# Kernel tuning notes

Hardware: AMD Instinct MI355X
Metric: run time of the kernel (lower is better)

## Reference

```python
import jax, jax.numpy as jnp
import numpy as np

B = 4; E_PER = 100_000; E = B * E_PER
N_NODES = 50_000; N_REL = 500; D = 64; D_LG = 256
K_PER_VI = 20; S_VI = E // K_PER_VI          # 20000 sorted vi segments
S_VJ_PER = 5_000; S_VJ = B * S_VJ_PER        # 20000 unsorted vj segments
N_MEM = 131_072
INTERACT = ((0, 3), (0, 2, 3), (0, 4), (0, 2, 4), (1, 3), (1, 2, 3), (1, 4), (1, 2, 4))


def _build_edges():
    rng = np.random.default_rng(0)
    idx_vi = np.repeat(np.arange(S_VI), K_PER_VI)          # sorted segment ids
    gpb = S_VI // B
    eg = idx_vi // gpb                                     # sorted by eg_idx too
    vi = rng.integers(0, N_NODES, S_VI)[idx_vi]
    idx_vj = np.empty(E, dtype=np.int64)
    for b in range(B):
        loc = np.concatenate([np.arange(S_VJ_PER), rng.integers(0, S_VJ_PER, E_PER - S_VJ_PER)])
        rng.shuffle(loc)
        idx_vj[b * E_PER:(b + 1) * E_PER] = b * S_VJ_PER + loc  # every group non-empty
    vj = rng.integers(0, N_NODES, S_VJ)[idx_vj]            # consistent (eg, vj) per group
    rel = rng.integers(0, N_REL, E)
    e2vi = rng.integers(0, N_MEM, E)
    e2vj = rng.integers(0, N_MEM, E)
    return np.stack([eg, vi, vj, rel, idx_vi, idx_vj, e2vi, e2vj], axis=1).astype(np.int32)


def setup_inputs() -> dict:
    key = jax.random.key(0)
    ks = jax.random.split(key, 10)
    return {
        "node_attention": jax.random.uniform(ks[0], (B, N_NODES), jnp.float32),
        "scanned_edges": jnp.asarray(_build_edges()),
        "edges_y": jax.random.uniform(ks[1], (E,), jnp.float32),
        "hidden_uncon": jax.random.normal(ks[2], (1, N_NODES, D_LG), jnp.float32),
        "hidden_con": jax.random.normal(ks[3], (N_MEM, D), jnp.float32),
        "Wc": jax.random.normal(ks[4], (D, D), jnp.float32) / np.sqrt(D).astype(np.float32),
        "bc": jnp.zeros((D,), jnp.float32),
        "Wu": jax.random.normal(ks[5], (D_LG, D), jnp.float32) / np.sqrt(D_LG).astype(np.float32),
        "bu": jnp.zeros((D,), jnp.float32),
        "rel_table": jax.random.normal(ks[6], (N_REL, D), jnp.float32) * 0.05,
        "ws": jax.random.normal(ks[7], (len(INTERACT), D), jnp.float32) / np.sqrt(float(len(INTERACT))).astype(np.float32) if False else jax.random.normal(ks[7], (len(INTERACT), D), jnp.float32) * (1.0 / np.sqrt(len(INTERACT)).astype(np.float32)),
        "fb": jnp.zeros((D,), jnp.float32),
        "out_w": jax.random.normal(ks[8], (D,), jnp.float32),
        "out_b": jnp.zeros((D,), jnp.float32),
        "n_vi_segments": S_VI,
        "n_vj_segments": S_VJ,
    }


def reference(node_attention, scanned_edges, edges_y, hidden_uncon, hidden_con,
              Wc, bc, Wu, bu, rel_table, ws, fb, out_w, out_b,
              n_vi_segments, n_vj_segments):
    eg, vi, vj, rel = (scanned_edges[:, i] for i in range(4))
    idx_vi, idx_vj, e2vi, e2vj = (scanned_edges[:, i] for i in range(4, 8))
    # projections (proj_con / proj_uncon, tanh Dense)
    hc = jnp.tanh(hidden_con @ Wc + bc)          # [N_MEM, D]
    hu = jnp.tanh(hidden_uncon @ Wu + bu)[0]     # [n_nodes, D]; batch_size==1 path of Node2Edge
    # Node2Edge gathers
    feats = (hc[e2vi], hu[vi], rel_table[rel], hc[e2vj], hu[vj])  # each [E, D]
    # F layer: weighted sum of elementwise interaction products
    out = fb
    for k, idxs in enumerate(INTERACT):
        x = feats[idxs[0]]
        for i in idxs[1:]:
            x = x * feats[i]
        out = out + x * ws[k]
    out = jax.nn.relu(out) * out_w + out_b
    logits = jnp.sum(out, axis=1)                # [E]
    # NeighborSoftmax at 'vi' (sorted segment softmax)
    m = jax.ops.segment_max(logits, idx_vi, num_segments=n_vi_segments)
    ex = jnp.exp(logits - m[idx_vi])
    den = jax.ops.segment_sum(ex, idx_vi, num_segments=n_vi_segments)
    transition = ex / den[idx_vi]
    # attention flow: gather source attention, weight, aggregate at vj
    trans_att = transition * node_attention[eg, vi] * edges_y
    aggr = jax.ops.segment_sum(trans_att, idx_vj, num_segments=n_vj_segments)
    b_g = jax.ops.segment_max(eg, idx_vj, num_segments=n_vj_segments)
    vj_g = jax.ops.segment_max(vj, idx_vj, num_segments=n_vj_segments)
    new_node_attention = jnp.zeros_like(node_attention).at[b_g, vj_g].add(aggr)
    return new_node_attention
```

## Files before the change

kernel.cpp:

```cpp
#include <hip/hip_runtime.h>
#include <hip/hip_bf16.h>
#include <type_traits>

#define D 64
#define KPER 20

typedef __attribute__((ext_vector_type(8))) short short8;
typedef __attribute__((ext_vector_type(4))) float floatx4;

__device__ __forceinline__ unsigned short f2bfu(float x) {
    __hip_bfloat16 h = __float2bfloat16(x);
    return *reinterpret_cast<unsigned short*>(&h);
}
__device__ __forceinline__ float bfu2f(unsigned short u) {
    return __uint_as_float(((unsigned)u) << 16);
}

__device__ __forceinline__ float fast_tanh(float x) {
    float xc = fminf(fmaxf(x, -15.f), 15.f);
    float e = __expf(2.f * xc);
    return 1.f - 2.f * __builtin_amdgcn_rcpf(1.f + e);
}

template<int CTRL>
__device__ __forceinline__ float dpp_add(float x) {
    int t = __builtin_amdgcn_update_dpp(0, __float_as_int(x), CTRL, 0xf, 0xf, true);
    return x + __int_as_float(t);
}
template<int CTRL>
__device__ __forceinline__ float dpp_max(float x) {
    int xi = __float_as_int(x);
    int t = __builtin_amdgcn_update_dpp(xi, xi, CTRL, 0xf, 0xf, false);
    return fmaxf(x, __int_as_float(t));
}
__device__ __forceinline__ float wave_sum_b(float x) {
    x = dpp_add<0x111>(x); x = dpp_add<0x112>(x);
    x = dpp_add<0x114>(x); x = dpp_add<0x118>(x);
    x = dpp_add<0x142>(x); x = dpp_add<0x143>(x);
    return __int_as_float(__builtin_amdgcn_readlane(__float_as_int(x), 63));
}
__device__ __forceinline__ float wave_max_b(float x) {
    x = dpp_max<0x111>(x); x = dpp_max<0x112>(x);
    x = dpp_max<0x114>(x); x = dpp_max<0x118>(x);
    x = dpp_max<0x142>(x); x = dpp_max<0x143>(x);
    return __int_as_float(__builtin_amdgcn_readlane(__float_as_int(x), 63));
}

template<int I, int N, typename F>
__device__ __forceinline__ void static_for(F&& f) {
    if constexpr (I < N) {
        f(std::integral_constant<int, I>{});
        static_for<I + 1, N>(f);
    }
}

template<int SLOT>
__device__ __forceinline__ int get_slot(int m0, int m1, int m2) {
    if constexpr (SLOT < 64)       return __builtin_amdgcn_readlane(m0, SLOT);
    else if constexpr (SLOT < 128) return __builtin_amdgcn_readlane(m1, SLOT - 64);
    else                           return __builtin_amdgcn_readlane(m2, SLOT - 128);
}

template<int K, int CTN>
__device__ __forceinline__ void proj_body(const float* __restrict__ h,
        const float* __restrict__ W, const float* __restrict__ b,
        unsigned short* __restrict__ out, int ct0, int rt0, int rtstride, int ntiles) {
    constexpr int KT = K / 32;
    int lane = threadIdx.x & 63;
    int m = lane & 15, quad = lane >> 4;
    short8 bfr[CTN][KT];
    #pragma unroll
    for (int ct = 0; ct < CTN; ++ct)
        #pragma unroll
        for (int kt = 0; kt < KT; ++kt)
            #pragma unroll
            for (int j = 0; j < 8; ++j)
                bfr[ct][kt][j] = (short)f2bfu(W[(size_t)(kt * 32 + quad * 8 + j) * 64 + (ct0 + ct) * 16 + m]);
    float bv[CTN];
    #pragma unroll
    for (int ct = 0; ct < CTN; ++ct) bv[ct] = b[(ct0 + ct) * 16 + m];
    for (int rt = rt0; rt < ntiles; rt += rtstride) {
        floatx4 acc[CTN];
        #pragma unroll
        for (int ct = 0; ct < CTN; ++ct) acc[ct] = floatx4{0.f, 0.f, 0.f, 0.f};
        const float* hrow = h + (size_t)(rt * 16 + m) * K + quad * 8;
        #pragma unroll
        for (int kt = 0; kt < KT; ++kt) {
            floatx4 a0 = *(const floatx4*)(hrow + kt * 32);
            floatx4 a1 = *(const floatx4*)(hrow + kt * 32 + 4);
            short8 af;
            af[0] = (short)f2bfu(a0[0]); af[1] = (short)f2bfu(a0[1]);
            af[2] = (short)f2bfu(a0[2]); af[3] = (short)f2bfu(a0[3]);
            af[4] = (short)f2bfu(a1[0]); af[5] = (short)f2bfu(a1[1]);
            af[6] = (short)f2bfu(a1[2]); af[7] = (short)f2bfu(a1[3]);
            #pragma unroll
            for (int ct = 0; ct < CTN; ++ct)
                acc[ct] = __builtin_amdgcn_mfma_f32_16x16x32_bf16(af, bfr[ct][kt], acc[ct], 0, 0, 0);
        }
        #pragma unroll
        for (int ct = 0; ct < CTN; ++ct) {
            int col = (ct0 + ct) * 16 + m;
            #pragma unroll
            for (int reg = 0; reg < 4; ++reg) {
                int row = rt * 16 + quad * 4 + reg;
                out[(size_t)row * 64 + col] = f2bfu(fast_tanh(acc[ct][reg] + bv[ct]));
            }
        }
    }
}

#define RELB 16
__global__ __launch_bounds__(256) void proj_fused(
        const float* __restrict__ hcon, const float* __restrict__ Wc, const float* __restrict__ bc,
        const float* __restrict__ hun, const float* __restrict__ Wu, const float* __restrict__ bu,
        const float* __restrict__ relf, unsigned short* __restrict__ hc,
        unsigned short* __restrict__ hu, unsigned short* __restrict__ relb,
        int t64, int t256, int g64, int g256, int nrel) {
    int bid = blockIdx.x;
    int w = threadIdx.x >> 6;
    if (bid < g64) {
        int wid = bid * 4 + w;
        proj_body<64, 4>(hcon, Wc, bc, hc, 0, wid, g64 * 4, t64);
    } else if (bid < g64 + g256) {
        int wid = (bid - g64) * 4 + w;
        int half = wid & 1;
        proj_body<256, 2>(hun, Wu, bu, hu, half * 2, wid >> 1, (g256 * 4) >> 1, t256);
    } else {
        int tid = (bid - g64 - g256) * 256 + threadIdx.x;
        for (int i = tid; i < nrel; i += RELB * 256) relb[i] = f2bfu(relf[i]);
    }
}

__global__ __launch_bounds__(256) void edge_kernel(
        const float* __restrict__ natt, const int* __restrict__ edges,
        const float* __restrict__ ey, const unsigned short* __restrict__ hc,
        const unsigned short* __restrict__ hu, const unsigned short* __restrict__ relt,
        const float* __restrict__ wsm, const float* __restrict__ fb,
        const float* __restrict__ outw, float* __restrict__ out, int N) {
    int lane = threadIdx.x & 63;
    int s = blockIdx.x * 4 + (threadIdx.x >> 6);
    long base = (long)s * KPER;
    const int* eb = edges + base * 8;
    int m0 = eb[lane];
    int m1 = eb[64 + lane];
    int m2 = (lane < 32) ? eb[128 + lane] : 0;
    int eg = get_slot<0>(m0, m1, m2);
    int vi = get_slot<1>(m0, m1, m2);
    float f1 = bfu2f(hu[(size_t)vi * D + lane]);
    float na = natt[(size_t)eg * N + vi];
    float w0 = wsm[0 * D + lane], w1 = wsm[1 * D + lane];
    float w2 = wsm[2 * D + lane], w3 = wsm[3 * D + lane];
    float w4 = wsm[4 * D + lane], w5 = wsm[5 * D + lane];
    float w6 = wsm[6 * D + lane], w7 = wsm[7 * D + lane];
    float fbv = fb[lane], owv = outw[lane];
    float myl = -INFINITY;
    int myvj = 0;
    static_for<0, KPER>([&](auto ec) {
        constexpr int e = decltype(ec)::value;
        int vj  = get_slot<e * 8 + 2>(m0, m1, m2);
        int rel = get_slot<e * 8 + 3>(m0, m1, m2);
        int evi = get_slot<e * 8 + 6>(m0, m1, m2);
        int evj = get_slot<e * 8 + 7>(m0, m1, m2);
        float F0 = bfu2f(hc[(size_t)evi * D + lane]);
        float F2 = bfu2f(relt[(size_t)rel * D + lane]);
        float F3 = bfu2f(hc[(size_t)evj * D + lane]);
        float F4 = bfu2f(hu[(size_t)vj * D + lane]);
        float t1 = fmaf(F2, w1, w0);
        float t2 = fmaf(F2, w5, w4);
        float t3 = fmaf(F2, w3, w2);
        float t4 = fmaf(F2, w7, w6);
        float u = fmaf(F0, t1, f1 * t2);
        float v = fmaf(F0, t3, f1 * t4);
        float o = fmaf(F3, u, fmaf(F4, v, fbv));
        o = fmaxf(o, 0.0f) * owv;
        float tot = wave_sum_b(o);
        bool mine = (lane == e);
        myl = mine ? tot : myl;
        myvj = mine ? vj : myvj;
    });
    float mx = wave_max_b(myl);
    float ex = __expf(myl - mx);
    float den = wave_sum_b(ex);
    if (lane < KPER) {
        float t = (ex / den) * na * ey[base + lane];
        atomicAdd(out + (size_t)eg * N + myvj, t);
    }
}

extern "C" void kernel_launch(void* const* d_in, const int* in_sizes, int n_in,
                              void* d_out, int out_size, void* d_ws, size_t ws_size,
                              hipStream_t stream) {
    const float* natt = (const float*)d_in[0];
    const int*   edges = (const int*)d_in[1];
    const float* ey   = (const float*)d_in[2];
    const float* hun  = (const float*)d_in[3];
    const float* hcon = (const float*)d_in[4];
    const float* Wc   = (const float*)d_in[5];
    const float* bc   = (const float*)d_in[6];
    const float* Wu   = (const float*)d_in[7];
    const float* bu   = (const float*)d_in[8];
    const float* relt = (const float*)d_in[9];
    const float* wsm  = (const float*)d_in[10];
    const float* fb   = (const float*)d_in[11];
    const float* outw = (const float*)d_in[12];
    float* out = (float*)d_out;

    int E    = in_sizes[2];
    int S    = E / KPER;
    int nmem = in_sizes[4] / D;
    int N    = in_sizes[3] / 256;
    int nrel = in_sizes[9];

    hipMemsetAsync(d_out, 0, (size_t)out_size * sizeof(float), stream);

    int t64  = nmem / 16;
    int t256 = N / 16;
    int g64  = 512, g256 = 512;

    unsigned short* hc = (unsigned short*)d_ws;
    unsigned short* hu = hc + (size_t)nmem * D;
    unsigned short* rb = hu + (size_t)N * D;

    proj_fused<<<g64 + g256 + RELB, 256, 0, stream>>>(hcon, Wc, bc, hun, Wu, bu,
                                                      relt, hc, hu, rb,
                                                      t64, t256, g64, g256, nrel);
    edge_kernel<<<S / 4, 256, 0, stream>>>(natt, edges, ey, hc, hu, rb,
                                           wsm, fb, outw, out, N);
}
```

Measured before the change: 207.2 us.

## Prefetch edge gathers, fold output zeroing into proj kernel, pair 64-dim tiles

The edge kernel now issues the four gathers for each edge three edges ahead, keeping them in a small rotating register buffer so that memory latency overlaps with the arithmetic and wave reductions. The separate hipMemsetAsync on the output is removed and replaced by extra blocks in the projection kernel that zero the output, which saves one launch. The 64-dim projection now gives each wave exactly two row tiles, with all loads issued up front and a grid sized to the tile count. In exchange, register pressure rises and the 64-dim path silently assumes nmem is divisible by 128.

Result: no change. 207.9 us (+0.4%).

```diff
diff --git a/kernel.cpp b/kernel.cpp
--- a/kernel.cpp
+++ b/kernel.cpp
@@ -61,11 +61,10 @@
     else                           return __builtin_amdgcn_readlane(m2, SLOT - 128);
 }
 
-template<int K, int CTN>
-__device__ __forceinline__ void proj_body(const float* __restrict__ h,
+__device__ __forceinline__ void proj64_pair(const float* __restrict__ h,
         const float* __restrict__ W, const float* __restrict__ b,
-        unsigned short* __restrict__ out, int ct0, int rt0, int rtstride, int ntiles) {
-    constexpr int KT = K / 32;
+        unsigned short* __restrict__ out, int rt0) {
+    constexpr int K = 64, KT = 2, CTN = 4;
     int lane = threadIdx.x & 63;
     int m = lane & 15, quad = lane >> 4;
     short8 bfr[CTN][KT];
@@ -75,31 +74,43 @@
         for (int kt = 0; kt < KT; ++kt)
             #pragma unroll
             for (int j = 0; j < 8; ++j)
-                bfr[ct][kt][j] = (short)f2bfu(W[(size_t)(kt * 32 + quad * 8 + j) * 64 + (ct0 + ct) * 16 + m]);
+                bfr[ct][kt][j] = (short)f2bfu(W[(size_t)(kt * 32 + quad * 8 + j) * 64 + ct * 16 + m]);
     float bv[CTN];
     #pragma unroll
-    for (int ct = 0; ct < CTN; ++ct) bv[ct] = b[(ct0 + ct) * 16 + m];
-    for (int rt = rt0; rt < ntiles; rt += rtstride) {
+    for (int ct = 0; ct < CTN; ++ct) bv[ct] = b[ct * 16 + m];
+    int rt1 = rt0 + 1;
+    const float* hrow0 = h + (size_t)(rt0 * 16 + m) * K + quad * 8;
+    const float* hrow1 = h + (size_t)(rt1 * 16 + m) * K + quad * 8;
+    floatx4 a0[KT][2], a1[KT][2];
+    #pragma unroll
+    for (int kt = 0; kt < KT; ++kt) {
+        a0[kt][0] = *(const floatx4*)(hrow0 + kt * 32);
+        a0[kt][1] = *(const floatx4*)(hrow0 + kt * 32 + 4);
+        a1[kt][0] = *(const floatx4*)(hrow1 + kt * 32);
+        a1[kt][1] = *(const floatx4*)(hrow1 + kt * 32 + 4);
+    }
+    #pragma unroll
+    for (int t = 0; t < 2; ++t) {
+        floatx4 (*ar)[2] = t ? a1 : a0;
+        int rt = t ? rt1 : rt0;
         floatx4 acc[CTN];
         #pragma unroll
         for (int ct = 0; ct < CTN; ++ct) acc[ct] = floatx4{0.f, 0.f, 0.f, 0.f};
-        const float* hrow = h + (size_t)(rt * 16 + m) * K + quad * 8;
         #pragma unroll
         for (int kt = 0; kt < KT; ++kt) {
-            floatx4 a0 = *(const floatx4*)(hrow + kt * 32);
-            floatx4 a1 = *(const floatx4*)(hrow + kt * 32 + 4);
             short8 af;
-            af[0] = (short)f2bfu(a0[0]); af[1] = (short)f2bfu(a0[1]);
-            af[2] = (short)f2bfu(a0[2]); af[3] = (short)f2bfu(a0[3]);
-            af[4] = (short)f2bfu(a1[0]); af[5] = (short)f2bfu(a1[1]);
-            af[6] = (short)f2bfu(a1[2]); af[7] = (short)f2bfu(a1[3]);
+            #pragma unroll
+            for (int j = 0; j < 4; ++j) {
+                af[j]     = (short)f2bfu(ar[kt][0][j]);
+                af[j + 4] = (short)f2bfu(ar[kt][1][j]);
+            }
             #pragma unroll
             for (int ct = 0; ct < CTN; ++ct)
                 acc[ct] = __builtin_amdgcn_mfma_f32_16x16x32_bf16(af, bfr[ct][kt], acc[ct], 0, 0, 0);
         }
         #pragma unroll
         for (int ct = 0; ct < CTN; ++ct) {
-            int col = (ct0 + ct) * 16 + m;
+            int col = ct * 16 + m;
             #pragma unroll
             for (int reg = 0; reg < 4; ++reg) {
                 int row = rt * 16 + quad * 4 + reg;
@@ -109,25 +120,78 @@
     }
 }
 
+__device__ __forceinline__ void proj256_body(const float* __restrict__ h,
+        const float* __restrict__ W, const float* __restrict__ b,
+        unsigned short* __restrict__ out, int ct0, int rt0, int rtstride, int ntiles) {
+    constexpr int K = 256, KT = 8, CTN = 2;
+    int lane = threadIdx.x & 63;
+    int m = lane & 15, quad = lane >> 4;
+    short8 bfr[CTN][KT];
+    #pragma unroll
+    for (int ct = 0; ct < CTN; ++ct)
+        #pragma unroll
+        for (int kt = 0; kt < KT; ++kt)
+            #pragma unroll
+            for (int j = 0; j < 8; ++j)
+                bfr[ct][kt][j] = (short)f2bfu(W[(size_t)(kt * 32 + quad * 8 + j) * 64 + (ct0 + ct) * 16 + m]);
+    float bv[CTN];
+    #pragma unroll
+    for (int ct = 0; ct < CTN; ++ct) bv[ct] = b[(ct0 + ct) * 16 + m];
+    for (int rt = rt0; rt < ntiles; rt += rtstride) {
+        floatx4 acc[CTN];
+        #pragma unroll
+        for (int ct = 0; ct < CTN; ++ct) acc[ct] = floatx4{0.f, 0.f, 0.f, 0.f};
+        const float* hrow = h + (size_t)(rt * 16 + m) * K + quad * 8;
+        #pragma unroll
+        for (int kt = 0; kt < KT; ++kt) {
+            floatx4 v0 = *(const floatx4*)(hrow + kt * 32);
+            floatx4 v1 = *(const floatx4*)(hrow + kt * 32 + 4);
+            short8 af;
+            #pragma unroll
+            for (int j = 0; j < 4; ++j) {
+                af[j]     = (short)f2bfu(v0[j]);
+                af[j + 4] = (short)f2bfu(v1[j]);
+            }
+            #pragma unroll
+            for (int ct = 0; ct < CTN; ++ct)
+                acc[ct] = __builtin_amdgcn_mfma_f32_16x16x32_bf16(af, bfr[ct][kt], acc[ct], 0, 0, 0);
+        }
+        #pragma unroll
+        for (int ct = 0; ct < CTN; ++ct) {
+            int col = (ct0 + ct) * 16 + m;
+            #pragma unroll
+            for (int reg = 0; reg < 4; ++reg) {
+                int row = rt * 16 + quad * 4 + reg;
+                out[(size_t)row * 64 + col] = f2bfu(fast_tanh(acc[ct][reg] + bv[ct]));
+            }
+        }
+    }
+}
+
 #define RELB 16
+#define ZB 8
 __global__ __launch_bounds__(256) void proj_fused(
         const float* __restrict__ hcon, const float* __restrict__ Wc, const float* __restrict__ bc,
         const float* __restrict__ hun, const float* __restrict__ Wu, const float* __restrict__ bu,
         const float* __restrict__ relf, unsigned short* __restrict__ hc,
         unsigned short* __restrict__ hu, unsigned short* __restrict__ relb,
+        float* __restrict__ outz, int nout,
         int t64, int t256, int g64, int g256, int nrel) {
     int bid = blockIdx.x;
     int w = threadIdx.x >> 6;
     if (bid < g64) {
         int wid = bid * 4 + w;
-        proj_body<64, 4>(hcon, Wc, bc, hc, 0, wid, g64 * 4, t64);
+        proj64_pair(hcon, Wc, bc, hc, wid * 2);
     } else if (bid < g64 + g256) {
         int wid = (bid - g64) * 4 + w;
         int half = wid & 1;
-        proj_body<256, 2>(hun, Wu, bu, hu, half * 2, wid >> 1, (g256 * 4) >> 1, t256);
-    } else {
+        proj256_body(hun, Wu, bu, hu, half * 2, wid >> 1, (g256 * 4) >> 1, t256);
+    } else if (bid < g64 + g256 + RELB) {
         int tid = (bid - g64 - g256) * 256 + threadIdx.x;
         for (int i = tid; i < nrel; i += RELB * 256) relb[i] = f2bfu(relf[i]);
+    } else {
+        int tid = (bid - g64 - g256 - RELB) * 256 + threadIdx.x;
+        for (int i = tid; i < nout; i += ZB * 256) outz[i] = 0.0f;
     }
 }
 
@@ -153,18 +217,35 @@
     float w4 = wsm[4 * D + lane], w5 = wsm[5 * D + lane];
     float w6 = wsm[6 * D + lane], w7 = wsm[7 * D + lane];
     float fbv = fb[lane], owv = outw[lane];
+
+    unsigned short F0r[4], F2r[4], F3r[4], F4r[4];
+    int vjr[4];
+    auto pref = [&](auto ec) {
+        constexpr int e = decltype(ec)::value;
+        constexpr int sl = e & 3;
+        int vj  = get_slot<e * 8 + 2>(m0, m1, m2);
+        int rel = get_slot<e * 8 + 3>(m0, m1, m2);
+        int evi = get_slot<e * 8 + 6>(m0, m1, m2);
+        int evj = get_slot<e * 8 + 7>(m0, m1, m2);
+        F0r[sl] = hc[(size_t)evi * D + lane];
+        F2r[sl] = relt[(size_t)rel * D + lane];
+        F3r[sl] = hc[(size_t)evj * D + lane];
+        F4r[sl] = hu[(size_t)vj * D + lane];
+        vjr[sl] = vj;
+    };
+    static_for<0, 3>(pref);
+
     float myl = -INFINITY;
     int myvj = 0;
     static_for<0, KPER>([&](auto ec) {
         constexpr int e = decltype(ec)::value;
-        int vj  = get_slot<e * 8 + 2>(m0, m1, m2);
-        int rel = get_slot<e * 8 + 3>(m0, m1, m2);
-        int evi = get_slot<e * 8 + 6>(m0, m1, m2);
-        int evj = get_slot<e * 8 + 7>(m0, m1, m2);
-        float F0 = bfu2f(hc[(size_t)evi * D + lane]);
-        float F2 = bfu2f(relt[(size_t)rel * D + lane]);
-        float F3 = bfu2f(hc[(size_t)evj * D + lane]);
-        float F4 = bfu2f(hu[(size_t)vj * D + lane]);
+        constexpr int sl = e & 3;
+        if constexpr (e + 3 < KPER) pref(std::integral_constant<int, e + 3>{});
+        float F0 = bfu2f(F0r[sl]);
+        float F2 = bfu2f(F2r[sl]);
+        float F3 = bfu2f(F3r[sl]);
+        float F4 = bfu2f(F4r[sl]);
+        int vj = vjr[sl];
         float t1 = fmaf(F2, w1, w0);
         float t2 = fmaf(F2, w5, w4);
         float t3 = fmaf(F2, w3, w2);
@@ -211,19 +292,19 @@
     int N    = in_sizes[3] / 256;
     int nrel = in_sizes[9];
 
-    hipMemsetAsync(d_out, 0, (size_t)out_size * sizeof(float), stream);
-
     int t64  = nmem / 16;
     int t256 = N / 16;
-    int g64  = 512, g256 = 512;
+    int g64  = t64 / 8;
+    int g256 = 512;
 
     unsigned short* hc = (unsigned short*)d_ws;
     unsigned short* hu = hc + (size_t)nmem * D;
     unsigned short* rb = hu + (size_t)N * D;
 
-    proj_fused<<<g64 + g256 + RELB, 256, 0, stream>>>(hcon, Wc, bc, hun, Wu, bu,
-                                                      relt, hc, hu, rb,
-                                                      t64, t256, g64, g256, nrel);
+    proj_fused<<<g64 + g256 + RELB + ZB, 256, 0, stream>>>(hcon, Wc, bc, hun, Wu, bu,
+                                                           relt, hc, hu, rb,
+                                                           out, out_size,
+                                                           t64, t256, g64, g256, nrel);
     edge_kernel<<<S / 4, 256, 0, stream>>>(natt, edges, ey, hc, hu, rb,
                                            wsm, fb, outw, out, N);
 }
```
